# Kernel tuning notes

Hardware: AMD Instinct MI355X
Metric: run time of the kernel (lower is better)

## Reference

```python
import jax, jax.numpy as jnp
import numpy as np

B, N, HID, HEADS, NCT, GDIM = 8, 1024, 1024, 16, 32, 128
HD = HID // HEADS  # head_dim = 64
SCALE = float(np.sqrt(HD))


def setup_inputs() -> dict:
    key = jax.random.key(0)
    ks = jax.random.split(key, 20)
    def lin(k, fan_in, shape):
        bound = 1.0 / np.sqrt(fan_in)
        return jax.random.uniform(k, shape, jnp.float32, -bound, bound)
    return {
        "x": jax.random.normal(ks[0], (B, N, HID), jnp.float32),
        "cancer_type": jax.random.randint(ks[1], (B,), 0, NCT),
        "graph_context": jax.random.normal(ks[2], (B, GDIM), jnp.float32),
        "attn_mask": jnp.zeros((B, N), dtype=bool),
        # projections (stored as [in, out] so y = x @ W + b)
        "Wq": lin(ks[3], HID, (HID, HID)), "bq": lin(ks[4], HID, (HID,)),
        "Wk": lin(ks[5], HID, (HID, HID)), "bk": lin(ks[6], HID, (HID,)),
        "Wv": lin(ks[7], HID, (HID, HID)), "bv": lin(ks[8], HID, (HID,)),
        "Wo": lin(ks[9], HID, (HID, HID)), "bo": lin(ks[10], HID, (HID,)),
        # embeddings
        "ct_bias_emb": jax.random.normal(ks[11], (NCT, HEADS), jnp.float32),
        "ct_key_emb": jax.random.normal(ks[12], (NCT, HID), jnp.float32),
        # graph_attn_bias MLP: graph_dim -> 2*heads -> heads (ELU between)
        "Wg1": lin(ks[13], GDIM, (GDIM, 2 * HEADS)), "bg1": lin(ks[14], GDIM, (2 * HEADS,)),
        "Wg2": lin(ks[15], 2 * HEADS, (2 * HEADS, HEADS)), "bg2": lin(ks[16], 2 * HEADS, (HEADS,)),
        # graph_key_mod: Linear(graph_dim, hidden) + ELU
        "Wgk": lin(ks[17], GDIM, (GDIM, HID)), "bgk": lin(ks[18], GDIM, (HID,)),
    }


def reference(x, cancer_type, graph_context, attn_mask,
              Wq, bq, Wk, bk, Wv, bv, Wo, bo,
              ct_bias_emb, ct_key_emb, Wg1, bg1, Wg2, bg2, Wgk, bgk):
    Bc, Nc, _ = x.shape
    # projections -> (B, H, N, D)
    def split_heads(t):
        return t.reshape(Bc, Nc, HEADS, HD).transpose(0, 2, 1, 3)
    q = split_heads(x @ Wq + bq)
    k = split_heads(x @ Wk + bk)
    v = split_heads(x @ Wv + bv)
    # additive key modulations, broadcast over N: (B, H, 1, D)
    ct_key = ct_key_emb[cancer_type].reshape(Bc, 1, HEADS, HD).transpose(0, 2, 1, 3)
    g_key = jax.nn.elu(graph_context @ Wgk + bgk).reshape(Bc, 1, HEADS, HD).transpose(0, 2, 1, 3)
    k = k + ct_key + g_key
    # scores (B, H, N, N)
    attn = jnp.einsum("bhqd,bhkd->bhqk", q, k) / SCALE
    ct_bias = ct_bias_emb[cancer_type]  # (B, H)
    g_bias = (jax.nn.elu(graph_context @ Wg1 + bg1) @ Wg2 + bg2)  # (B, H)
    attn = attn + (ct_bias + g_bias)[:, :, None, None]
    attn = jnp.where(attn_mask[:, None, None, :], -jnp.inf, attn)
    attn = jax.nn.softmax(attn, axis=-1)
    out = jnp.einsum("bhqk,bhkd->bhqd", attn, v)
    out = out.transpose(0, 2, 1, 3).reshape(Bc, Nc, HID)
    return out @ Wo + bo
```

## Files before the change

kernel.cpp:

```cpp
#include <hip/hip_runtime.h>

typedef unsigned short u16;
typedef __attribute__((ext_vector_type(4))) unsigned short u16x4;
typedef __attribute__((ext_vector_type(2))) unsigned u32x2;
typedef __attribute__((ext_vector_type(8))) __bf16 bf16x8;
typedef __attribute__((ext_vector_type(2))) __bf16 bf16x2;
typedef __attribute__((ext_vector_type(4))) float f32x4;

#define DEV __device__ __forceinline__

DEV u16 f2b(float f) {
    union { float f; unsigned u; } v; v.f = f;
    unsigned r = v.u + 0x7FFFu + ((v.u >> 16) & 1u);
    return (u16)(r >> 16);
}
DEV unsigned pk2(float a, float b) {
    bf16x2 t; t.x = (__bf16)a; t.y = (__bf16)b;
    union { bf16x2 v; unsigned u; } c; c.v = t; return c.u;
}
DEV u16 cvt1(float f) {
    __bf16 h = (__bf16)f;
    union { __bf16 h; u16 u; } c; c.h = h; return c.u;
}

DEV void gl_lds16(const u16* g, const u16* l) {
    __builtin_amdgcn_global_load_lds(
        (__attribute__((address_space(1))) void*)(unsigned long long)g,
        (__attribute__((address_space(3))) void*)(unsigned long long)l,
        16, 0, 0);
}

DEV void sync_keep4() {
    asm volatile("s_waitcnt vmcnt(4)" ::: "memory");
    __builtin_amdgcn_s_barrier();
    asm volatile("" ::: "memory");
}
DEV void sync_keep5() {
    asm volatile("s_waitcnt vmcnt(5)" ::: "memory");
    __builtin_amdgcn_s_barrier();
    asm volatile("" ::: "memory");
}
DEV void sync_drain() {
    asm volatile("s_waitcnt vmcnt(0)" ::: "memory");
    __builtin_amdgcn_s_barrier();
    asm volatile("" ::: "memory");
}

__global__ __launch_bounds__(256) void k_prep(const float* __restrict__ xf, u16* __restrict__ xb,
                                              const float* w0, const float* w1,
                                              const float* w2, const float* w3,
                                              u16* __restrict__ dst)
{
    __shared__ u16 t[64][68];
    int bx = blockIdx.x;
    if (bx < 8192) {
        size_t base = (size_t)bx * 1024 + threadIdx.x * 4;
        float4 v = *(const float4*)&xf[base];
        u16x4 o; o.x = f2b(v.x); o.y = f2b(v.y); o.z = f2b(v.z); o.w = f2b(v.w);
        *(u16x4*)&xb[base] = o;
        return;
    }
    bx -= 8192;
    int z = bx >> 8, tile = bx & 255;
    const float* src = z == 0 ? w0 : z == 1 ? w1 : z == 2 ? w2 : w3;
    u16* d = dst + (size_t)z * 1048576;
    int tx = threadIdx.x & 15, ty = threadIdx.x >> 4;
    int c0 = (tile & 15) * 64, r0 = (tile >> 4) * 64;
#pragma unroll
    for (int i = 0; i < 4; i++) {
        int r = ty + i * 16;
        float4 v = *(const float4*)&src[(size_t)(r0 + r) * 1024 + c0 + tx * 4];
        t[r][tx * 4 + 0] = f2b(v.x); t[r][tx * 4 + 1] = f2b(v.y);
        t[r][tx * 4 + 2] = f2b(v.z); t[r][tx * 4 + 3] = f2b(v.w);
    }
    __syncthreads();
#pragma unroll
    for (int i = 0; i < 4; i++) {
        int cl = ty + i * 16;
        u16x4 v;
        v.x = t[tx * 4 + 0][cl];
        v.y = t[tx * 4 + 1][cl];
        v.z = t[tx * 4 + 2][cl];
        v.w = t[tx * 4 + 3][cl];
        *(u16x4*)&d[(size_t)(c0 + cl) * 1024 + r0 + tx * 4] = v;
    }
}

__global__ __launch_bounds__(256, 2) void k_qkvf(const u16* __restrict__ x, const u16* __restrict__ WT,
                                                 const float* __restrict__ bq, const float* __restrict__ bk,
                                                 const float* __restrict__ bv,
                                                 u16* __restrict__ QK, u16* __restrict__ Vt)
{
    __shared__ u16 lds[40960];
    const int tid = threadIdx.x;
    const int w = tid >> 6, lane = tid & 63, quad = lane >> 4, l16 = lane & 15;
    const int wr = w >> 1, wc = w & 1;
    const int m0 = blockIdx.y * 128, n0 = blockIdx.x * 64;
    const int K = 1024;

    f32x4 acc[3][4][2] = {};

    int srowA[2], skofA[2];
#pragma unroll
    for (int ph = 0; ph < 2; ph++) {
        int L = (ph * 256 + tid) * 8;
        int pr = L >> 6, cp = (L >> 3) & 7;
        int c = cp ^ (pr & 7);
        srowA[ph] = pr * 2 + (c >> 2); skofA[ph] = (c & 3) * 8;
    }
    int LB = tid * 8;
    int prB = LB >> 6, cpB = (LB >> 3) & 7;
    int cB = cpB ^ (prB & 7);
    int srowB = prB * 2 + (cB >> 2), skofB = (cB & 3) * 8;

    const u16* Ap0 = x + ((size_t)m0 + srowA[0]) * K + skofA[0];
    const u16* Ap1 = x + ((size_t)m0 + srowA[1]) * K + skofA[1];
    const u16* Bp0 = WT + ((size_t)n0 + srowB) * K + skofB;
    const u16* Bp1 = Bp0 + (size_t)1048576;
    const u16* Bp2 = Bp0 + (size_t)2097152;
    const int wof = w * 512;

    auto STAGE = [&](int pb, int t, int kh) {
        size_t ko = (size_t)t * 64 + kh * 32;
        int la = pb * 8192 + kh * 4096 + wof;
        gl_lds16(Ap0 + ko, lds + la);
        gl_lds16(Ap1 + ko, lds + la + 2048);
        int lb = 16384 + pb * 4096 + kh * 2048 + wof;
        gl_lds16(Bp0 + ko, lds + lb);
        gl_lds16(Bp1 + ko, lds + lb + 8192);
        gl_lds16(Bp2 + ko, lds + lb + 16384);
    };

    int aoff[4], boff[2];
#pragma unroll
    for (int mi = 0; mi < 4; mi++) {
        int row = wr * 64 + mi * 16 + l16;
        aoff[mi] = (row >> 1) * 64 + (((((row & 1) << 2) | quad) ^ ((row >> 1) & 7)) << 3);
    }
#pragma unroll
    for (int ni = 0; ni < 2; ni++) {
        int r = wc * 32 + ni * 16 + l16;
        boff[ni] = (r >> 1) * 64 + (((((r & 1) << 2) | quad) ^ ((r >> 1) & 7)) << 3);
    }

    auto LOADF = [&](int pb, int kh, bf16x8 (&a)[4], bf16x8 (&b)[3][2]) {
        const u16* Ab = lds + pb * 8192 + kh * 4096;
        const u16* Bb = lds + 16384 + pb * 4096 + kh * 2048;
#pragma unroll
        for (int mi = 0; mi < 4; mi++) a[mi] = *(const bf16x8*)&Ab[aoff[mi]];
#pragma unroll
        for (int m = 0; m < 3; m++)
#pragma unroll
            for (int ni = 0; ni < 2; ni++)
                b[m][ni] = *(const bf16x8*)&Bb[m * 8192 + boff[ni]];
    };

    auto MM = [&](const bf16x8 (&a)[4], const bf16x8 (&b)[3][2]) {
        __builtin_amdgcn_s_setprio(1);
#pragma unroll
        for (int m = 0; m < 3; m++)
#pragma unroll
            for (int mi = 0; mi < 4; mi++)
#pragma unroll
                for (int ni = 0; ni < 2; ni++)
                    acc[m][mi][ni] = __builtin_amdgcn_mfma_f32_16x16x32_bf16(a[mi], b[m][ni], acc[m][mi][ni], 0, 0, 0);
        __builtin_amdgcn_s_setprio(0);
    };

    STAGE(0, 0, 0);
    STAGE(0, 0, 1);
    sync_keep5();

    const int NT = 16;
    for (int t = 0; t < NT - 1; ++t) {
        const int p = t & 1, qb = p ^ 1;
        bf16x8 a[4], b[3][2];
        LOADF(p, 0, a, b);
        STAGE(qb, t + 1, 0);
        sync_keep5();
        MM(a, b);
        LOADF(p, 1, a, b);
        STAGE(qb, t + 1, 1);
        sync_keep5();
        MM(a, b);
    }
    {
        const int p = (NT - 1) & 1;
        bf16x8 a[4], b[3][2];
        LOADF(p, 0, a, b);
        sync_drain();
        MM(a, b);
        LOADF(p, 1, a, b);
        MM(a, b);
    }

    float bsq[2], bsk[2], bsv2[2];
#pragma unroll
    for (int ni = 0; ni < 2; ni++) {
        int col = n0 + wc * 32 + ni * 16 + l16;
        bsq[ni] = bq[col]; bsk[ni] = bk[col]; bsv2[ni] = bv[col];
    }

#pragma unroll
    for (int mi = 0; mi < 4; mi++) {
        int row = m0 + wr * 64 + mi * 16 + quad * 4;
#pragma unroll
        for (int ni = 0; ni < 2; ni++) {
            int col = n0 + wc * 32 + ni * 16 + l16;
#pragma unroll
            for (int r2 = 0; r2 < 4; r2++) {
                QK[(size_t)(row + r2) * 1024 + col] =
                    f2b((acc[0][mi][ni][r2] + bsq[ni]) * 0.18033688011f);
                QK[(size_t)8388608 + (size_t)(row + r2) * 1024 + col] =
                    f2b(acc[1][mi][ni][r2] + bsk[ni]);
            }
        }
    }
    {
        int bb = m0 >> 10, nbase = (m0 & 1023) + wr * 64;
#pragma unroll
        for (int mi = 0; mi < 4; mi++) {
            int nrow = nbase + mi * 16 + quad * 4;
#pragma unroll
            for (int ni = 0; ni < 2; ni++) {
                int col = n0 + wc * 32 + ni * 16 + l16;
                int hh = col >> 6, dd = col & 63;
                u16x4 pk;
                pk.x = f2b(acc[2][mi][ni][0] + bsv2[ni]);
                pk.y = f2b(acc[2][mi][ni][1] + bsv2[ni]);
                pk.z = f2b(acc[2][mi][ni][2] + bsv2[ni]);
                pk.w = f2b(acc[2][mi][ni][3] + bsv2[ni]);
                *(u16x4*)&Vt[(size_t)(bb * 16 + hh) * 65536 + (size_t)dd * 1024 + nrow] = pk;
            }
        }
    }
}

__global__ __launch_bounds__(256, 2) void k_out4(const u16* __restrict__ A, const u16* __restrict__ WoT,
                                                 const float* __restrict__ bo, float* __restrict__ C)
{
    __shared__ u16 lds[32768];
    const int tid = threadIdx.x;
    const int w = tid >> 6, lane = tid & 63, quad = lane >> 4, l16 = lane & 15;
    const int wr = w >> 1, wc = w & 1;
    const int m0 = blockIdx.y * 128, n0 = blockIdx.x * 128;
    const int K = 1024;

    f32x4 acc[4][4] = {};

    int srowA[2], skofA[2];
#pragma unroll
    for (int ph = 0; ph < 2; ph++) {
        int L = (ph * 256 + tid) * 8;
        int pr = L >> 6, cp = (L >> 3) & 7;
        int c = cp ^ (pr & 7);
        srowA[ph] = pr * 2 + (c >> 2); skofA[ph] = (c & 3) * 8;
    }
    const u16* Ap0 = A + ((size_t)m0 + srowA[0]) * K + skofA[0];
    const u16* Ap1 = A + ((size_t)m0 + srowA[1]) * K + skofA[1];
    const u16* Bq0 = WoT + ((size_t)n0 + srowA[0]) * K + skofA[0];
    const u16* Bq1 = WoT + ((size_t)n0 + srowA[1]) * K + skofA[1];
    const int wof = w * 512;

    auto STAGE = [&](int pb, int t, int kh) {
        size_t ko = (size_t)t * 64 + kh * 32;
        int la = pb * 8192 + kh * 4096 + wof;
        gl_lds16(Ap0 + ko, lds + la);
        gl_lds16(Ap1 + ko, lds + la + 2048);
        gl_lds16(Bq0 + ko, lds + 16384 + la);
        gl_lds16(Bq1 + ko, lds + 16384 + la + 2048);
    };

    int aoff[4], boff[4];
#pragma unroll
    for (int mi = 0; mi < 4; mi++) {
        int row = wr * 64 + mi * 16 + l16;
        aoff[mi] = (row >> 1) * 64 + (((((row & 1) << 2) | quad) ^ ((row >> 1) & 7)) << 3);
    }
#pragma unroll
    for (int ni = 0; ni < 4; ni++) {
        int r = wc * 64 + ni * 16 + l16;
        boff[ni] = (r >> 1) * 64 + (((((r & 1) << 2) | quad) ^ ((r >> 1) & 7)) << 3);
    }

    auto LOADF = [&](int pb, int kh, bf16x8 (&a)[4], bf16x8 (&b)[4]) {
        const u16* Ab = lds + pb * 8192 + kh * 4096;
        const u16* Bb = lds + 16384 + pb * 8192 + kh * 4096;
#pragma unroll
        for (int mi = 0; mi < 4; mi++) a[mi] = *(const bf16x8*)&Ab[aoff[mi]];
#pragma unroll
        for (int ni = 0; ni < 4; ni++) b[ni] = *(const bf16x8*)&Bb[boff[ni]];
    };

    auto MM = [&](const bf16x8 (&a)[4], const bf16x8 (&b)[4]) {
        __builtin_amdgcn_s_setprio(1);
#pragma unroll
        for (int mi = 0; mi < 4; mi++)
#pragma unroll
            for (int ni = 0; ni < 4; ni++)
                acc[mi][ni] = __builtin_amdgcn_mfma_f32_16x16x32_bf16(a[mi], b[ni], acc[mi][ni], 0, 0, 0);
        __builtin_amdgcn_s_setprio(0);
    };

    STAGE(0, 0, 0);
    STAGE(0, 0, 1);
    sync_keep4();

    const int NT = 16;
    for (int t = 0; t < NT - 1; ++t) {
        const int p = t & 1, qb = p ^ 1;
        bf16x8 a[4], b[4];
        LOADF(p, 0, a, b);
        STAGE(qb, t + 1, 0);
        sync_keep4();
        MM(a, b);
        LOADF(p, 1, a, b);
        STAGE(qb, t + 1, 1);
        sync_keep4();
        MM(a, b);
    }
    {
        const int p = (NT - 1) & 1;
        bf16x8 a[4], b[4];
        LOADF(p, 0, a, b);
        sync_drain();
        MM(a, b);
        LOADF(p, 1, a, b);
        MM(a, b);
    }

    float bs[4];
#pragma unroll
    for (int ni = 0; ni < 4; ni++)
        bs[ni] = bo[n0 + wc * 64 + ni * 16 + l16];
#pragma unroll
    for (int mi = 0; mi < 4; mi++) {
        int row = m0 + wr * 64 + mi * 16 + quad * 4;
#pragma unroll
        for (int ni = 0; ni < 4; ni++) {
            int col = n0 + wc * 64 + ni * 16 + l16;
#pragma unroll
            for (int r2 = 0; r2 < 4; r2++)
                C[(size_t)(row + r2) * 1024 + col] = acc[mi][ni][r2] + bs[ni];
        }
    }
}

__global__ __launch_bounds__(256, 4) void k_attn(const u16* __restrict__ Q, const u16* __restrict__ K,
                                                 const u16* __restrict__ Vt, u16* __restrict__ O)
{
    __shared__ u16 lds[13312];
    const int tid = threadIdx.x, w = tid >> 6, lane = tid & 63, quad = lane >> 4, l16 = lane & 15;
    const int bh = blockIdx.y, b = bh >> 4, h = bh & 15;
    const int q0 = blockIdx.x * 128;
    const u16* Qp = Q + ((size_t)b * 1024 + q0) * 1024 + h * 64;
    const u16* Kp = K + (size_t)b * 1048576 + h * 64;
    const u16* Vp = Vt + (size_t)bh * 65536;
    u16* Op = O + ((size_t)b * 1024 + q0) * 1024 + h * 64;
    u16* Pw = lds + 8192 + w * 1280;

#pragma unroll
    for (int i = 0; i < 4; i++) {
        int g = (w * 4 + i) * 64 + lane;
        int row = g >> 3, c = (g & 7) ^ (row & 7);
        gl_lds16(Qp + (size_t)row * 1024 + c * 8, lds + (w * 4 + i) * 512);
    }
    __syncthreads();
    bf16x8 qa[2][2];
#pragma unroll
    for (int ni = 0; ni < 2; ni++)
#pragma unroll
        for (int d2 = 0; d2 < 2; d2++)
            qa[ni][d2] = *(const bf16x8*)&lds[(w * 32 + ni * 16 + l16) * 64 + ((d2 * 4 + quad) ^ (l16 & 7)) * 8];
    __syncthreads();

    {
        int g = w * 64 + lane;
        int row = g >> 3, c = (g & 7) ^ (row & 7);
        gl_lds16(Kp + (size_t)row * 1024 + c * 8, lds + w * 512);
        int rv = g >> 2, cv = (g & 3) ^ (rv & 3);
        gl_lds16(Vp + (size_t)rv * 1024 + cv * 8, lds + 2048 + w * 512);
    }
    __syncthreads();

    bf16x8 ones;
#pragma unroll
    for (int j = 0; j < 8; j++) ones[j] = (__bf16)1.0f;

    f32x4 acc_o[2][4] = {};
    f32x4 acc_l[2] = {};

    for (int kt = 0; kt < 32; kt++) {
        const u16* buf = lds + (kt & 1) * 4096;
        if (kt < 31) {
            int k0n = (kt + 1) * 32;
            u16* dst = lds + ((kt + 1) & 1) * 4096;
            int g = w * 64 + lane;
            int row = g >> 3, c = (g & 7) ^ (row & 7);
            gl_lds16(Kp + (size_t)(k0n + row) * 1024 + c * 8, dst + w * 512);
            int rv = g >> 2, cv = (g & 3) ^ (rv & 3);
            gl_lds16(Vp + (size_t)rv * 1024 + k0n + cv * 8, dst + 2048 + w * 512);
        }

        f32x4 s[2][2] = {};
#pragma unroll
        for (int d2 = 0; d2 < 2; d2++) {
            bf16x8 ka[2];
#pragma unroll
            for (int mi = 0; mi < 2; mi++)
                ka[mi] = *(const bf16x8*)&buf[(mi * 16 + l16) * 64 + ((d2 * 4 + quad) ^ (l16 & 7)) * 8];
#pragma unroll
            for (int mi = 0; mi < 2; mi++)
#pragma unroll
                for (int ni = 0; ni < 2; ni++)
                    s[mi][ni] = __builtin_amdgcn_mfma_f32_16x16x32_bf16(ka[mi], qa[ni][d2], s[mi][ni], 0, 0, 0);
        }

#pragma unroll
        for (int ni = 0; ni < 2; ni++)
#pragma unroll
            for (int mi = 0; mi < 2; mi++) {
                float e0 = __builtin_amdgcn_exp2f(s[mi][ni][0]);
                float e1 = __builtin_amdgcn_exp2f(s[mi][ni][1]);
                float e2 = __builtin_amdgcn_exp2f(s[mi][ni][2]);
                float e3 = __builtin_amdgcn_exp2f(s[mi][ni][3]);
                u32x2 pk; pk.x = pk2(e0, e1); pk.y = pk2(e2, e3);
                *(u32x2*)&Pw[(ni * 16 + l16) * 40 + mi * 16 + quad * 4] = pk;
            }

        {
            bf16x8 pa[2], vb[4];
#pragma unroll
            for (int ni = 0; ni < 2; ni++)
                pa[ni] = *(const bf16x8*)&Pw[(ni * 16 + l16) * 40 + quad * 8];
#pragma unroll
            for (int di = 0; di < 4; di++)
                vb[di] = *(const bf16x8*)&buf[2048 + (di * 16 + l16) * 32 + (quad ^ (l16 & 3)) * 8];
#pragma unroll
            for (int ni = 0; ni < 2; ni++) {
                acc_l[ni] = __builtin_amdgcn_mfma_f32_16x16x32_bf16(pa[ni], ones, acc_l[ni], 0, 0, 0);
#pragma unroll
                for (int di = 0; di < 4; di++)
                    acc_o[ni][di] = __builtin_amdgcn_mfma_f32_16x16x32_bf16(pa[ni], vb[di], acc_o[ni][di], 0, 0, 0);
            }
        }
        __syncthreads();
    }

#pragma unroll
    for (int ni = 0; ni < 2; ni++) {
#pragma unroll
        for (int r = 0; r < 4; r++) {
            float inv = __builtin_amdgcn_rcpf(acc_l[ni][r]);
            int row = w * 32 + ni * 16 + quad * 4 + r;
#pragma unroll
            for (int di = 0; di < 4; di++)
                Op[(size_t)row * 1024 + di * 16 + l16] = cvt1(acc_o[ni][di][r] * inv);
        }
    }
}

extern "C" void kernel_launch(void* const* d_in, const int* in_sizes, int n_in,
                              void* d_out, int out_size, void* d_ws, size_t ws_size,
                              hipStream_t stream)
{
    (void)in_sizes; (void)n_in; (void)out_size; (void)ws_size;
    const float* xf  = (const float*)d_in[0];
    const float* Wqf = (const float*)d_in[4];  const float* bqf = (const float*)d_in[5];
    const float* Wkf = (const float*)d_in[6];  const float* bkf = (const float*)d_in[7];
    const float* Wvf = (const float*)d_in[8];  const float* bvf = (const float*)d_in[9];
    const float* Wof = (const float*)d_in[10]; const float* bof = (const float*)d_in[11];

    u16* ws  = (u16*)d_ws;
    u16* Qw  = ws;
    u16* Kw  = ws + (size_t)8388608;
    u16* Vtw = ws + (size_t)16777216;
    u16* WT  = ws + (size_t)25165824;
    u16* xb  = ws + (size_t)29360128;
    u16* AO  = xb;

    k_prep<<<9216, 256, 0, stream>>>(xf, xb, Wqf, Wkf, Wvf, Wof, WT);
    k_qkvf<<<dim3(16, 64), 256, 0, stream>>>(xb, WT, bqf, bkf, bvf, Qw, Vtw);
    k_attn<<<dim3(8, 128), 256, 0, stream>>>(Qw, Kw, Vtw, AO);
    k_out4<<<dim3(8, 64), 256, 0, stream>>>(AO, WT + (size_t)3145728, bof, (float*)d_out);
}
```

Before: 253.7 us.

## Load QKV weight fragments directly from global into registers, stage only activations in LDS

The fused QKV GEMM now stages only the activation tile through LDS. The three weight matrices' fragments are read straight from global memory into registers, double-buffered across half-K steps, and the vmcnt waits are retuned for the changed number of outstanding loads. This shrinks LDS from 80KB to 32KB per block, which may allow more resident blocks, and removes the LDS write/read round trip for B. The cost is uncoalesced 16-byte-per-lane global loads, higher register pressure, and exposed global latency on the weight path.

```diff
diff --git a/kernel.cpp b/kernel.cpp
--- a/kernel.cpp
+++ b/kernel.cpp
@@ -35,8 +35,13 @@
     __builtin_amdgcn_s_barrier();
     asm volatile("" ::: "memory");
 }
-DEV void sync_keep5() {
-    asm volatile("s_waitcnt vmcnt(5)" ::: "memory");
+DEV void sync_keep6() {
+    asm volatile("s_waitcnt vmcnt(6)" ::: "memory");
+    __builtin_amdgcn_s_barrier();
+    asm volatile("" ::: "memory");
+}
+DEV void sync_keep8() {
+    asm volatile("s_waitcnt vmcnt(8)" ::: "memory");
     __builtin_amdgcn_s_barrier();
     asm volatile("" ::: "memory");
 }
@@ -91,7 +96,7 @@
                                                  const float* __restrict__ bv,
                                                  u16* __restrict__ QK, u16* __restrict__ Vt)
 {
-    __shared__ u16 lds[40960];
+    __shared__ u16 lds[16384];
     const int tid = threadIdx.x;
     const int w = tid >> 6, lane = tid & 63, quad = lane >> 4, l16 = lane & 15;
     const int wr = w >> 1, wc = w & 1;
@@ -108,53 +113,44 @@
         int c = cp ^ (pr & 7);
         srowA[ph] = pr * 2 + (c >> 2); skofA[ph] = (c & 3) * 8;
     }
-    int LB = tid * 8;
-    int prB = LB >> 6, cpB = (LB >> 3) & 7;
-    int cB = cpB ^ (prB & 7);
-    int srowB = prB * 2 + (cB >> 2), skofB = (cB & 3) * 8;
-
     const u16* Ap0 = x + ((size_t)m0 + srowA[0]) * K + skofA[0];
     const u16* Ap1 = x + ((size_t)m0 + srowA[1]) * K + skofA[1];
-    const u16* Bp0 = WT + ((size_t)n0 + srowB) * K + skofB;
-    const u16* Bp1 = Bp0 + (size_t)1048576;
-    const u16* Bp2 = Bp0 + (size_t)2097152;
     const int wof = w * 512;
 
-    auto STAGE = [&](int pb, int t, int kh) {
+    auto STAGE_A = [&](int pb, int t, int kh) {
         size_t ko = (size_t)t * 64 + kh * 32;
         int la = pb * 8192 + kh * 4096 + wof;
         gl_lds16(Ap0 + ko, lds + la);
         gl_lds16(Ap1 + ko, lds + la + 2048);
-        int lb = 16384 + pb * 4096 + kh * 2048 + wof;
-        gl_lds16(Bp0 + ko, lds + lb);
-        gl_lds16(Bp1 + ko, lds + lb + 8192);
-        gl_lds16(Bp2 + ko, lds + lb + 16384);
-    };
-
-    int aoff[4], boff[2];
+    };
+
+    int aoff[4];
 #pragma unroll
     for (int mi = 0; mi < 4; mi++) {
         int row = wr * 64 + mi * 16 + l16;
         aoff[mi] = (row >> 1) * 64 + (((((row & 1) << 2) | quad) ^ ((row >> 1) & 7)) << 3);
     }
-#pragma unroll
-    for (int ni = 0; ni < 2; ni++) {
-        int r = wc * 32 + ni * 16 + l16;
-        boff[ni] = (r >> 1) * 64 + (((((r & 1) << 2) | quad) ^ ((r >> 1) & 7)) << 3);
-    }
-
-    auto LOADF = [&](int pb, int kh, bf16x8 (&a)[4], bf16x8 (&b)[3][2]) {
+
+    const u16* bbase[3][2];
+#pragma unroll
+    for (int m = 0; m < 3; m++)
+#pragma unroll
+        for (int ni = 0; ni < 2; ni++)
+            bbase[m][ni] = WT + (size_t)m * 1048576
+                         + (size_t)(n0 + wc * 32 + ni * 16 + l16) * 1024 + quad * 8;
+
+    auto LOADA = [&](int pb, int kh, bf16x8 (&a)[4]) {
         const u16* Ab = lds + pb * 8192 + kh * 4096;
-        const u16* Bb = lds + 16384 + pb * 4096 + kh * 2048;
 #pragma unroll
         for (int mi = 0; mi < 4; mi++) a[mi] = *(const bf16x8*)&Ab[aoff[mi]];
+    };
+    auto LOADB = [&](int koff, bf16x8 (&b)[3][2]) {
 #pragma unroll
         for (int m = 0; m < 3; m++)
 #pragma unroll
             for (int ni = 0; ni < 2; ni++)
-                b[m][ni] = *(const bf16x8*)&Bb[m * 8192 + boff[ni]];
-    };
-
+                b[m][ni] = *(const bf16x8*)(bbase[m][ni] + koff);
+    };
     auto MM = [&](const bf16x8 (&a)[4], const bf16x8 (&b)[3][2]) {
         __builtin_amdgcn_s_setprio(1);
 #pragma unroll
@@ -167,31 +163,41 @@
         __builtin_amdgcn_s_setprio(0);
     };
 
-    STAGE(0, 0, 0);
-    STAGE(0, 0, 1);
-    sync_keep5();
+    bf16x8 b0[3][2], b1[3][2];
+
+    LOADB(0, b0);
+    STAGE_A(0, 0, 0);
+    STAGE_A(0, 0, 1);
+    sync_drain();
 
     const int NT = 16;
     for (int t = 0; t < NT - 1; ++t) {
         const int p = t & 1, qb = p ^ 1;
-        bf16x8 a[4], b[3][2];
-        LOADF(p, 0, a, b);
-        STAGE(qb, t + 1, 0);
-        sync_keep5();
-        MM(a, b);
-        LOADF(p, 1, a, b);
-        STAGE(qb, t + 1, 1);
-        sync_keep5();
-        MM(a, b);
+        {
+            bf16x8 a[4];
+            LOADA(p, 0, a);
+            STAGE_A(qb, t + 1, 0);
+            sync_keep8();
+            MM(a, b0);
+            LOADB(t * 64 + 32, b1);
+        }
+        {
+            bf16x8 a[4];
+            LOADA(p, 1, a);
+            STAGE_A(qb, t + 1, 1);
+            sync_keep8();
+            MM(a, b1);
+            LOADB((t + 1) * 64, b0);
+        }
     }
     {
-        const int p = (NT - 1) & 1;
-        bf16x8 a[4], b[3][2];
-        LOADF(p, 0, a, b);
-        sync_drain();
-        MM(a, b);
-        LOADF(p, 1, a, b);
-        MM(a, b);
+        bf16x8 a[4];
+        LOADA(1, 0, a);
+        sync_keep6();
+        MM(a, b0);
+        LOADB(15 * 64 + 32, b1);
+        LOADA(1, 1, a);
+        MM(a, b1);
     }
 
     float bsq[2], bsk[2], bsv2[2];
```

After: 299.7 us. 1.18x slower.
